# Optimization experiments

Measured on AMD Instinct MI355X. Metric: run time of the kernel, lower is better.

The kernel has to match this reference:

```python
import jax, jax.numpy as jnp
import numpy as np
from itertools import combinations_with_replacement

LATENT_DIM = 16
N_PARAMS = 2
N_VARS = LATENT_DIM + N_PARAMS  # 18
POLY_ORDER = 3
BATCH = 131072

# Static exponent index tables: for each degree d, an [n_terms_d, d] array of
# variable indices (combinations with replacement), matching a sympy-style
# polynomial library [1, x_i, x_i*x_j, x_i*x_j*x_k, ...].
IDX = [np.array(list(combinations_with_replacement(range(N_VARS), d)), dtype=np.int32)
       for d in range(1, POLY_ORDER + 1)]
P = 1 + sum(a.shape[0] for a in IDX)  # 1330 library terms


def setup_inputs() -> dict:
    key = jax.random.key(0)
    k1, k2, k3 = jax.random.split(key, 3)
    z = jax.random.normal(k1, (BATCH, LATENT_DIM), dtype=jnp.float32)
    betas = jax.random.normal(k2, (BATCH, N_PARAMS), dtype=jnp.float32)
    big_xi = jax.random.normal(k3, (P, N_VARS), dtype=jnp.float32) * 0.1
    mask = jnp.ones((P, N_VARS), dtype=jnp.float32)
    return {"z": z, "betas": betas, "big_xi": big_xi, "mask": mask}


def _theta(x):
    # x: [B, N_VARS] -> theta: [B, P]
    cols = [jnp.ones((x.shape[0], 1), dtype=x.dtype)]  # constant term
    for idx in IDX:
        acc = x[:, idx[:, 0]]                # [B, n_terms_d]
        for k in range(1, idx.shape[1]):     # loop over degree (<= POLY_ORDER)
            acc = acc * x[:, idx[:, k]]
        cols.append(acc)
    return jnp.concatenate(cols, axis=1)


def reference(z, betas, big_xi, mask):
    x = jnp.concatenate([z, betas], axis=1)  # [B, N_VARS]
    theta = _theta(x)                        # [B, P]
    return theta @ (big_xi * mask)           # [B, N_VARS]
```

## Files before the change

### kernel.cpp

```cpp
#include <hip/hip_runtime.h>
#include <hip/hip_bf16.h>
#include <utility>


constexpr int NVARS   = 18;
constexpr int NOUT    = 18;
constexpr int NROWS   = 131072;
constexpr int NCHUNKS = 43;
constexpr int NSLOTS  = NCHUNKS * 8;

constexpr int WF0_SHORTS = NCHUNKS * 512;
constexpr int WF1_SHORTS = NCHUNKS * 72;
constexpr int WF_SHORTS  = WF0_SHORTS + WF1_SHORTS;
constexpr int LDS_SHORTS = 28672;

typedef __attribute__((ext_vector_type(8))) short short8;
typedef __attribute__((ext_vector_type(4))) float f32x4;
typedef __attribute__((ext_vector_type(2))) float f32x2;

struct T3 { int a, b, c; };

constexpr int rho1(int v) {
    if (v < 16)  return (v & ~3) | ((v + 1) & 3);
    if (v == 16) return 17;
    if (v == 17) return 16;
    return v;
}
constexpr int rho2v(int v) { return rho1(rho1(v)); }

constexpr T3 sort3(int u0, int u1, int u2) {
    int t = 0;
    if (u0 > u1) { t = u0; u0 = u1; u1 = t; }
    if (u1 > u2) { t = u1; u1 = u2; u2 = t; }
    if (u0 > u1) { t = u0; u0 = u1; u1 = t; }
    return T3{u0, u1, u2};
}
constexpr T3 rho3(T3 t) { return sort3(rho1(t.a), rho1(t.b), rho1(t.c)); }

constexpr bool t3_less(T3 x, T3 y) {
    if (x.a != y.a) return x.a < y.a;
    if (x.b != y.b) return x.b < y.b;
    return x.c < y.c;
}
constexpr bool t3_eq(T3 x, T3 y) { return x.a == y.a && x.b == y.b && x.c == y.c; }

constexpr int rank_of(T3 t) {
    int deg = (t.a < 18) + (t.b < 18) + (t.c < 18);
    if (deg == 0) return 0;
    if (deg == 1) return 1 + t.a;
    if (deg == 2) {
        int r = 19;
        for (int a = 0; a < t.a; ++a) r += 18 - a;
        return r + (t.b - t.a);
    }
    int r = 190;
    for (int a = 0; a < t.a; ++a) { int n = 18 - a; r += n * (n + 1) / 2; }
    for (int b = t.a; b < t.b; ++b) r += 18 - b;
    return r + (t.c - t.b);
}

struct RepTables {
    signed char va[NSLOTS], vb[NSLOTS], vc[NSLOTS];
    short p[4][NSLOTS];
    int count;
};

constexpr void consider(RepTables& R, int& s, T3 t) {
    T3 im[4] = {t, T3{0, 0, 0}, T3{0, 0, 0}, T3{0, 0, 0}};
    im[1] = rho3(im[0]);
    im[2] = rho3(im[1]);
    im[3] = rho3(im[2]);
    for (int g = 1; g < 4; ++g)
        if (t3_less(im[g], t)) return;
    R.va[s] = (signed char)t.a; R.vb[s] = (signed char)t.b; R.vc[s] = (signed char)t.c;
    for (int g = 0; g < 4; ++g) {
        bool dup = false;
        for (int h = 0; h < g; ++h)
            if (t3_eq(im[h], im[g])) dup = true;
        R.p[g][s] = dup ? (short)-1 : (short)rank_of(im[g]);
    }
    ++s;
}

constexpr RepTables make_tables() {
    RepTables R{};
    int s = 0;
    consider(R, s, T3{18, 18, 18});
    for (int a = 0; a < NVARS; ++a) consider(R, s, T3{a, 18, 18});
    for (int a = 0; a < NVARS; ++a)
        for (int b = a; b < NVARS; ++b) consider(R, s, T3{a, b, 18});
    for (int a = 0; a < NVARS; ++a)
        for (int b = a; b < NVARS; ++b)
            for (int c = b; c < NVARS; ++c) consider(R, s, T3{a, b, c});
    R.count = s;
    for (; s < NSLOTS; ++s) {
        R.va[s] = 19; R.vb[s] = 19; R.vc[s] = 19;
        for (int g = 0; g < 4; ++g) R.p[g][s] = -1;
    }
    return R;
}

constexpr RepTables h_tab = make_tables();
static_assert(h_tab.count == 342, "orbit enumeration must give 342 rep slots");
__device__ const RepTables d_tab = make_tables();

__device__ __align__(16) short g_wf[WF_SHORTS];


#if __has_builtin(__builtin_amdgcn_cvt_pk_bf16_f32)
typedef __bf16 bf16x2 __attribute__((ext_vector_type(2)));
__device__ __forceinline__ unsigned pack2(float f0, float f1) {
    bf16x2 r = __builtin_amdgcn_cvt_pk_bf16_f32(f0, f1);
    return __builtin_bit_cast(unsigned, r);
}
#else
__device__ __forceinline__ unsigned pack2(float f0, float f1) {
    unsigned u0 = __float_as_uint(f0) + 0x8000u;
    unsigned u1 = __float_as_uint(f1) + 0x8000u;
    return __builtin_amdgcn_perm(u1, u0, 0x07060302u);
}
#endif


template <int S>
__device__ __forceinline__ f32x2 term_val2(const f32x2 (&x)[NVARS]) {
    constexpr int a = h_tab.va[S], b = h_tab.vb[S], c = h_tab.vc[S];
    if constexpr (a >= 19)      return f32x2{0.0f, 0.0f};
    else if constexpr (a == 18) return f32x2{1.0f, 1.0f};
    else if constexpr (b == 18) return x[a];
    else if constexpr (c == 18) return x[a] * x[b];
    else                        return x[a] * x[b] * x[c];
}

union AFrag { unsigned u[4]; short8 v; };

template <int CI, int... I>
__device__ __forceinline__ void eval8(const f32x2 (&x)[NVARS], f32x2 (&t)[8],
                                      std::integer_sequence<int, I...>) {
    ((t[I] = term_val2<CI * 8 + I>(x)), ...);
}

template <int CI>
__device__ __forceinline__ void kstep(const f32x2 (&x)[NVARS],
                                      const short* p0, const short* p1,
                                      f32x4& acc00, f32x4& acc01,
                                      f32x4& acc10, f32x4& acc11) {
    f32x2 t[8];
    eval8<CI>(x, t, std::make_integer_sequence<int, 8>{});
    AFrag afA, afB;
#pragma unroll
    for (int j = 0; j < 4; ++j) {
        afA.u[j] = pack2(t[2 * j][0], t[2 * j + 1][0]);
        afB.u[j] = pack2(t[2 * j][1], t[2 * j + 1][1]);
    }
    short8 b0 = *(const short8*)(p0 + CI * 512);
    short8 b1 = *(const short8*)(p1 + CI * 72);
    acc00 = __builtin_amdgcn_mfma_f32_16x16x32_bf16(afA.v, b0, acc00, 0, 0, 0);
    acc10 = __builtin_amdgcn_mfma_f32_16x16x32_bf16(afB.v, b0, acc10, 0, 0, 0);
    acc01 = __builtin_amdgcn_mfma_f32_16x16x32_bf16(afA.v, b1, acc01, 0, 0, 0);
    acc11 = __builtin_amdgcn_mfma_f32_16x16x32_bf16(afB.v, b1, acc11, 0, 0, 0);
}

template <int... CI>
__device__ __forceinline__ void kloop(const f32x2 (&x)[NVARS],
                                      const short* p0, const short* p1,
                                      f32x4& acc00, f32x4& acc01,
                                      f32x4& acc10, f32x4& acc11,
                                      std::integer_sequence<int, CI...>) {
    (kstep<CI>(x, p0, p1, acc00, acc01, acc10, acc11), ...);
}

__device__ __forceinline__ void load_x(const float* __restrict__ z,
                                       const float* __restrict__ betas,
                                       int arow, bool s1, bool s2, float (&x)[NVARS]) {
    float x0[NVARS];
    const float4* z4 = (const float4*)(z + (size_t)arow * 16);
    float4 v0 = z4[0], v1 = z4[1], v2 = z4[2], v3 = z4[3];
    x0[0]  = v0.x; x0[1]  = v0.y; x0[2]  = v0.z; x0[3]  = v0.w;
    x0[4]  = v1.x; x0[5]  = v1.y; x0[6]  = v1.z; x0[7]  = v1.w;
    x0[8]  = v2.x; x0[9]  = v2.y; x0[10] = v2.z; x0[11] = v2.w;
    x0[12] = v3.x; x0[13] = v3.y; x0[14] = v3.z; x0[15] = v3.w;
    const float2 b2 = *(const float2*)(betas + (size_t)arow * 2);
    x0[16] = b2.x; x0[17] = b2.y;
    float y[NVARS];
#pragma unroll
    for (int v = 0; v < NVARS; ++v) y[v] = s1 ? x0[rho1(v)] : x0[v];
#pragma unroll
    for (int v = 0; v < NVARS; ++v) x[v] = s2 ? y[rho2v(v)] : y[v];
}

__global__ __launch_bounds__(512)
__attribute__((amdgpu_waves_per_eu(4, 4)))
void vindy_mfma(const float* __restrict__ z,
                const float* __restrict__ betas,
                float* __restrict__ out) {
    __shared__ __align__(16) short ldsW[LDS_SHORTS];

    {
        const float4* src = (const float4*)g_wf;
        float4* dst = (float4*)ldsW;
        for (int i = threadIdx.x; i < WF_SHORTS / 8; i += 512) dst[i] = src[i];
    }
    __syncthreads();

    const int lane = threadIdx.x & 63;
    const int wave = threadIdx.x >> 6;
    const int g    = lane >> 4;
    const int n    = lane & 15;
    const int rowbase = blockIdx.x * 256 + wave * 32;

    const bool s1 = (g & 1) != 0;
    const bool s2 = (g & 2) != 0;
    float xA[NVARS], xB[NVARS];
    load_x(z, betas, rowbase + n,      s1, s2, xA);
    load_x(z, betas, rowbase + 16 + n, s1, s2, xB);
    f32x2 x[NVARS];
#pragma unroll
    for (int v = 0; v < NVARS; ++v) x[v] = f32x2{xA[v], xB[v]};

    const short* p0 = ldsW + lane * 8;
    const short* p1 = ldsW + WF0_SHORTS + (n < 2 ? (g * 2 + n) * 8 : 64);

    f32x4 acc00, acc01, acc10, acc11;
#pragma unroll
    for (int i = 0; i < 4; ++i) { acc00[i] = 0.0f; acc01[i] = 0.0f; acc10[i] = 0.0f; acc11[i] = 0.0f; }

    kloop(x, p0, p1, acc00, acc01, acc10, acc11,
          std::make_integer_sequence<int, NCHUNKS>{});

    float* o0 = out + (size_t)(rowbase + g * 4) * NOUT;
    float* o1 = out + (size_t)(rowbase + 16 + g * 4) * NOUT;
#pragma unroll
    for (int r = 0; r < 4; ++r) {
        o0[(size_t)r * NOUT + n] = acc00[r];
        o1[(size_t)r * NOUT + n] = acc10[r];
    }
    if (n < 2) {
#pragma unroll
        for (int r = 0; r < 4; ++r) {
            o0[(size_t)r * NOUT + 16 + n] = acc01[r];
            o1[(size_t)r * NOUT + 16 + n] = acc11[r];
        }
    }
}


__global__ void prep_wfrag(const float* __restrict__ xi, const float* __restrict__ mask) {
    int i = blockIdx.x * blockDim.x + threadIdx.x;
    if (i >= WF_SHORTS) return;
    float v = 0.0f;
    if (i < WF0_SHORTS) {
        int j = i & 7, l = (i >> 3) & 63, c = i >> 9;
        int col = l & 15;
        int p = d_tab.p[l >> 4][c * 8 + j];
        if (p >= 0) v = xi[p * NOUT + col] * mask[p * NOUT + col];
    } else {
        int i2 = i - WF0_SHORTS;
        int c = i2 / 72;
        int r = i2 - c * 72;
        int q = r >> 3, j = r & 7;
        if (q < 8) {
            int col = 16 + (q & 1);
            int p = d_tab.p[q >> 1][c * 8 + j];
            if (p >= 0) v = xi[p * NOUT + col] * mask[p * NOUT + col];
        }
    }
    g_wf[i] = __builtin_bit_cast(short, __float2bfloat16(v));
}

extern "C" void kernel_launch(void* const* d_in, const int* in_sizes, int n_in,
                              void* d_out, int out_size, void* d_ws, size_t ws_size,
                              hipStream_t stream) {
    const float* z     = (const float*)d_in[0];
    const float* betas = (const float*)d_in[1];
    const float* xi    = (const float*)d_in[2];
    const float* mask  = (const float*)d_in[3];
    float* out = (float*)d_out;
    (void)d_ws; (void)ws_size;

    prep_wfrag<<<(WF_SHORTS + 255) / 256, 256, 0, stream>>>(xi, mask);
    vindy_mfma<<<NROWS / 256, 512, 0, stream>>>(z, betas, out);
}
```

Before: 96.98 us.

## Process one 16-row tile per pass to reduce register pressure

Replaces the paired two-tile evaluation (f32x2 values and four MFMA accumulators) with a runtime loop over two single-tile passes, each using two accumulators. The waves_per_eu hint is removed and LDS is sized exactly to the weight fragments. The aim is lower VGPR usage and more scheduling freedom, at the cost of losing packed dual-row arithmetic and the MFMA interleaving that hid latency.

New measurement: 183.6 us. 89.3% more time.

```diff
diff --git a/kernel.cpp b/kernel.cpp
--- a/kernel.cpp
+++ b/kernel.cpp
@@ -12,11 +12,9 @@
 constexpr int WF0_SHORTS = NCHUNKS * 512;
 constexpr int WF1_SHORTS = NCHUNKS * 72;
 constexpr int WF_SHORTS  = WF0_SHORTS + WF1_SHORTS;
-constexpr int LDS_SHORTS = 28672;
 
 typedef __attribute__((ext_vector_type(8))) short short8;
 typedef __attribute__((ext_vector_type(4))) float f32x4;
-typedef __attribute__((ext_vector_type(2))) float f32x2;
 
 struct T3 { int a, b, c; };
 
@@ -123,10 +121,10 @@
 
 
 template <int S>
-__device__ __forceinline__ f32x2 term_val2(const f32x2 (&x)[NVARS]) {
+__device__ __forceinline__ float term_val(const float (&x)[NVARS]) {
     constexpr int a = h_tab.va[S], b = h_tab.vb[S], c = h_tab.vc[S];
-    if constexpr (a >= 19)      return f32x2{0.0f, 0.0f};
-    else if constexpr (a == 18) return f32x2{1.0f, 1.0f};
+    if constexpr (a >= 19)      return 0.0f;
+    else if constexpr (a == 18) return 1.0f;
     else if constexpr (b == 18) return x[a];
     else if constexpr (c == 18) return x[a] * x[b];
     else                        return x[a] * x[b] * x[c];
@@ -135,39 +133,32 @@
 union AFrag { unsigned u[4]; short8 v; };
 
 template <int CI, int... I>
-__device__ __forceinline__ void eval8(const f32x2 (&x)[NVARS], f32x2 (&t)[8],
+__device__ __forceinline__ void eval8(const float (&x)[NVARS], float (&t)[8],
                                       std::integer_sequence<int, I...>) {
-    ((t[I] = term_val2<CI * 8 + I>(x)), ...);
+    ((t[I] = term_val<CI * 8 + I>(x)), ...);
 }
 
 template <int CI>
-__device__ __forceinline__ void kstep(const f32x2 (&x)[NVARS],
+__device__ __forceinline__ void kstep(const float (&x)[NVARS],
                                       const short* p0, const short* p1,
-                                      f32x4& acc00, f32x4& acc01,
-                                      f32x4& acc10, f32x4& acc11) {
-    f32x2 t[8];
+                                      f32x4& acc0, f32x4& acc1) {
+    float t[8];
     eval8<CI>(x, t, std::make_integer_sequence<int, 8>{});
-    AFrag afA, afB;
-#pragma unroll
-    for (int j = 0; j < 4; ++j) {
-        afA.u[j] = pack2(t[2 * j][0], t[2 * j + 1][0]);
-        afB.u[j] = pack2(t[2 * j][1], t[2 * j + 1][1]);
-    }
+    AFrag af;
+#pragma unroll
+    for (int j = 0; j < 4; ++j) af.u[j] = pack2(t[2 * j], t[2 * j + 1]);
     short8 b0 = *(const short8*)(p0 + CI * 512);
     short8 b1 = *(const short8*)(p1 + CI * 72);
-    acc00 = __builtin_amdgcn_mfma_f32_16x16x32_bf16(afA.v, b0, acc00, 0, 0, 0);
-    acc10 = __builtin_amdgcn_mfma_f32_16x16x32_bf16(afB.v, b0, acc10, 0, 0, 0);
-    acc01 = __builtin_amdgcn_mfma_f32_16x16x32_bf16(afA.v, b1, acc01, 0, 0, 0);
-    acc11 = __builtin_amdgcn_mfma_f32_16x16x32_bf16(afB.v, b1, acc11, 0, 0, 0);
+    acc0 = __builtin_amdgcn_mfma_f32_16x16x32_bf16(af.v, b0, acc0, 0, 0, 0);
+    acc1 = __builtin_amdgcn_mfma_f32_16x16x32_bf16(af.v, b1, acc1, 0, 0, 0);
 }
 
 template <int... CI>
-__device__ __forceinline__ void kloop(const f32x2 (&x)[NVARS],
+__device__ __forceinline__ void kloop(const float (&x)[NVARS],
                                       const short* p0, const short* p1,
-                                      f32x4& acc00, f32x4& acc01,
-                                      f32x4& acc10, f32x4& acc11,
+                                      f32x4& acc0, f32x4& acc1,
                                       std::integer_sequence<int, CI...>) {
-    (kstep<CI>(x, p0, p1, acc00, acc01, acc10, acc11), ...);
+    (kstep<CI>(x, p0, p1, acc0, acc1), ...);
 }
 
 __device__ __forceinline__ void load_x(const float* __restrict__ z,
@@ -189,12 +180,11 @@
     for (int v = 0; v < NVARS; ++v) x[v] = s2 ? y[rho2v(v)] : y[v];
 }
 
-__global__ __launch_bounds__(512)
-__attribute__((amdgpu_waves_per_eu(4, 4)))
-void vindy_mfma(const float* __restrict__ z,
-                const float* __restrict__ betas,
-                float* __restrict__ out) {
-    __shared__ __align__(16) short ldsW[LDS_SHORTS];
+__global__ __launch_bounds__(512) void vindy_mfma(const float* __restrict__ z,
+                                                  const float* __restrict__ betas,
+                                                  float* __restrict__ out,
+                                                  int npass) {
+    __shared__ __align__(16) short ldsW[WF_SHORTS];
 
     {
         const float4* src = (const float4*)g_wf;
@@ -211,35 +201,27 @@
 
     const bool s1 = (g & 1) != 0;
     const bool s2 = (g & 2) != 0;
-    float xA[NVARS], xB[NVARS];
-    load_x(z, betas, rowbase + n,      s1, s2, xA);
-    load_x(z, betas, rowbase + 16 + n, s1, s2, xB);
-    f32x2 x[NVARS];
-#pragma unroll
-    for (int v = 0; v < NVARS; ++v) x[v] = f32x2{xA[v], xB[v]};
 
     const short* p0 = ldsW + lane * 8;
     const short* p1 = ldsW + WF0_SHORTS + (n < 2 ? (g * 2 + n) * 8 : 64);
 
-    f32x4 acc00, acc01, acc10, acc11;
-#pragma unroll
-    for (int i = 0; i < 4; ++i) { acc00[i] = 0.0f; acc01[i] = 0.0f; acc10[i] = 0.0f; acc11[i] = 0.0f; }
-
-    kloop(x, p0, p1, acc00, acc01, acc10, acc11,
-          std::make_integer_sequence<int, NCHUNKS>{});
-
-    float* o0 = out + (size_t)(rowbase + g * 4) * NOUT;
-    float* o1 = out + (size_t)(rowbase + 16 + g * 4) * NOUT;
-#pragma unroll
-    for (int r = 0; r < 4; ++r) {
-        o0[(size_t)r * NOUT + n] = acc00[r];
-        o1[(size_t)r * NOUT + n] = acc10[r];
-    }
-    if (n < 2) {
-#pragma unroll
-        for (int r = 0; r < 4; ++r) {
-            o0[(size_t)r * NOUT + 16 + n] = acc01[r];
-            o1[(size_t)r * NOUT + 16 + n] = acc11[r];
+    for (int half = 0; half < npass; ++half) {
+        const int row0 = rowbase + half * 16;
+        float x[NVARS];
+        load_x(z, betas, row0 + n, s1, s2, x);
+
+        f32x4 acc0, acc1;
+#pragma unroll
+        for (int i = 0; i < 4; ++i) { acc0[i] = 0.0f; acc1[i] = 0.0f; }
+
+        kloop(x, p0, p1, acc0, acc1, std::make_integer_sequence<int, NCHUNKS>{});
+
+        float* o = out + (size_t)(row0 + g * 4) * NOUT;
+#pragma unroll
+        for (int r = 0; r < 4; ++r) o[(size_t)r * NOUT + n] = acc0[r];
+        if (n < 2) {
+#pragma unroll
+            for (int r = 0; r < 4; ++r) o[(size_t)r * NOUT + 16 + n] = acc1[r];
         }
     }
 }
@@ -279,5 +261,5 @@
     (void)d_ws; (void)ws_size;
 
     prep_wfrag<<<(WF_SHORTS + 255) / 256, 256, 0, stream>>>(xi, mask);
-    vindy_mfma<<<NROWS / 256, 512, 0, stream>>>(z, betas, out);
-}
+    vindy_mfma<<<NROWS / 256, 512, 0, stream>>>(z, betas, out, 2);
+}
```

## Switch to scalar term evaluation and 1024-thread blocks

Applied to the files above, without the earlier changes.

Term evaluation now works on two separate scalar float arrays instead of packed float2 vectors, likely so the compiler can allocate registers more freely or avoid packed-math overhead. Blocks grow from 512 to 1024 threads, covering 512 rows each. This halves the number of per-block LDS weight copies, and the launch bounds move from an explicit waves-per-EU attribute to a (1024,4) hint. Packed v_pk_mul instructions may be lost, doubling the VALU multiply count, and the larger blocks change occupancy and scheduling granularity. The LDS allocation size also grows, though the data copied into it does not.

After: 104.1 us. 1.07x slower.

```diff
diff --git a/kernel.cpp b/kernel.cpp
--- a/kernel.cpp
+++ b/kernel.cpp
@@ -12,11 +12,10 @@
 constexpr int WF0_SHORTS = NCHUNKS * 512;
 constexpr int WF1_SHORTS = NCHUNKS * 72;
 constexpr int WF_SHORTS  = WF0_SHORTS + WF1_SHORTS;
-constexpr int LDS_SHORTS = 28672;
+constexpr int LDS_SHORTS = 41472;
 
 typedef __attribute__((ext_vector_type(8))) short short8;
 typedef __attribute__((ext_vector_type(4))) float f32x4;
-typedef __attribute__((ext_vector_type(2))) float f32x2;
 
 struct T3 { int a, b, c; };
 
@@ -123,10 +122,10 @@
 
 
 template <int S>
-__device__ __forceinline__ f32x2 term_val2(const f32x2 (&x)[NVARS]) {
+__device__ __forceinline__ float term_val(const float (&x)[NVARS]) {
     constexpr int a = h_tab.va[S], b = h_tab.vb[S], c = h_tab.vc[S];
-    if constexpr (a >= 19)      return f32x2{0.0f, 0.0f};
-    else if constexpr (a == 18) return f32x2{1.0f, 1.0f};
+    if constexpr (a >= 19)      return 0.0f;
+    else if constexpr (a == 18) return 1.0f;
     else if constexpr (b == 18) return x[a];
     else if constexpr (c == 18) return x[a] * x[b];
     else                        return x[a] * x[b] * x[c];
@@ -135,23 +134,24 @@
 union AFrag { unsigned u[4]; short8 v; };
 
 template <int CI, int... I>
-__device__ __forceinline__ void eval8(const f32x2 (&x)[NVARS], f32x2 (&t)[8],
+__device__ __forceinline__ void eval8(const float (&x)[NVARS], float (&t)[8],
                                       std::integer_sequence<int, I...>) {
-    ((t[I] = term_val2<CI * 8 + I>(x)), ...);
+    ((t[I] = term_val<CI * 8 + I>(x)), ...);
 }
 
 template <int CI>
-__device__ __forceinline__ void kstep(const f32x2 (&x)[NVARS],
+__device__ __forceinline__ void kstep(const float (&xA)[NVARS], const float (&xB)[NVARS],
                                       const short* p0, const short* p1,
                                       f32x4& acc00, f32x4& acc01,
                                       f32x4& acc10, f32x4& acc11) {
-    f32x2 t[8];
-    eval8<CI>(x, t, std::make_integer_sequence<int, 8>{});
+    float tA[8], tB[8];
+    eval8<CI>(xA, tA, std::make_integer_sequence<int, 8>{});
+    eval8<CI>(xB, tB, std::make_integer_sequence<int, 8>{});
     AFrag afA, afB;
 #pragma unroll
     for (int j = 0; j < 4; ++j) {
-        afA.u[j] = pack2(t[2 * j][0], t[2 * j + 1][0]);
-        afB.u[j] = pack2(t[2 * j][1], t[2 * j + 1][1]);
+        afA.u[j] = pack2(tA[2 * j], tA[2 * j + 1]);
+        afB.u[j] = pack2(tB[2 * j], tB[2 * j + 1]);
     }
     short8 b0 = *(const short8*)(p0 + CI * 512);
     short8 b1 = *(const short8*)(p1 + CI * 72);
@@ -162,12 +162,12 @@
 }
 
 template <int... CI>
-__device__ __forceinline__ void kloop(const f32x2 (&x)[NVARS],
+__device__ __forceinline__ void kloop(const float (&xA)[NVARS], const float (&xB)[NVARS],
                                       const short* p0, const short* p1,
                                       f32x4& acc00, f32x4& acc01,
                                       f32x4& acc10, f32x4& acc11,
                                       std::integer_sequence<int, CI...>) {
-    (kstep<CI>(x, p0, p1, acc00, acc01, acc10, acc11), ...);
+    (kstep<CI>(xA, xB, p0, p1, acc00, acc01, acc10, acc11), ...);
 }
 
 __device__ __forceinline__ void load_x(const float* __restrict__ z,
@@ -189,17 +189,15 @@
     for (int v = 0; v < NVARS; ++v) x[v] = s2 ? y[rho2v(v)] : y[v];
 }
 
-__global__ __launch_bounds__(512)
-__attribute__((amdgpu_waves_per_eu(4, 4)))
-void vindy_mfma(const float* __restrict__ z,
-                const float* __restrict__ betas,
-                float* __restrict__ out) {
+__global__ __launch_bounds__(1024, 4) void vindy_mfma(const float* __restrict__ z,
+                                                      const float* __restrict__ betas,
+                                                      float* __restrict__ out) {
     __shared__ __align__(16) short ldsW[LDS_SHORTS];
 
     {
         const float4* src = (const float4*)g_wf;
         float4* dst = (float4*)ldsW;
-        for (int i = threadIdx.x; i < WF_SHORTS / 8; i += 512) dst[i] = src[i];
+        for (int i = threadIdx.x; i < WF_SHORTS / 8; i += 1024) dst[i] = src[i];
     }
     __syncthreads();
 
@@ -207,16 +205,13 @@
     const int wave = threadIdx.x >> 6;
     const int g    = lane >> 4;
     const int n    = lane & 15;
-    const int rowbase = blockIdx.x * 256 + wave * 32;
+    const int rowbase = blockIdx.x * 512 + wave * 32;
 
     const bool s1 = (g & 1) != 0;
     const bool s2 = (g & 2) != 0;
     float xA[NVARS], xB[NVARS];
     load_x(z, betas, rowbase + n,      s1, s2, xA);
     load_x(z, betas, rowbase + 16 + n, s1, s2, xB);
-    f32x2 x[NVARS];
-#pragma unroll
-    for (int v = 0; v < NVARS; ++v) x[v] = f32x2{xA[v], xB[v]};
 
     const short* p0 = ldsW + lane * 8;
     const short* p1 = ldsW + WF0_SHORTS + (n < 2 ? (g * 2 + n) * 8 : 64);
@@ -225,7 +220,7 @@
 #pragma unroll
     for (int i = 0; i < 4; ++i) { acc00[i] = 0.0f; acc01[i] = 0.0f; acc10[i] = 0.0f; acc11[i] = 0.0f; }
 
-    kloop(x, p0, p1, acc00, acc01, acc10, acc11,
+    kloop(xA, xB, p0, p1, acc00, acc01, acc10, acc11,
           std::make_integer_sequence<int, NCHUNKS>{});
 
     float* o0 = out + (size_t)(rowbase + g * 4) * NOUT;
@@ -279,5 +274,5 @@
     (void)d_ws; (void)ws_size;
 
     prep_wfrag<<<(WF_SHORTS + 255) / 256, 256, 0, stream>>>(xi, mask);
-    vindy_mfma<<<NROWS / 256, 512, 0, stream>>>(z, betas, out);
-}
+    vindy_mfma<<<NROWS / 512, 1024, 0, stream>>>(z, betas, out);
+}
```
